# Kernel tuning notes

Measured on AMD Instinct MI355X. Metric: run time of the kernel, lower is better.

Reference implementation:

```python
import jax, jax.numpy as jnp
import numpy as np

N, E, G = 50000, 800000, 64
IN_C, HID, HEADS = 128, 64, 4
NEG_SLOPE = 0.2


def setup_inputs() -> dict:
    key = jax.random.key(0)
    ks = jax.random.split(key, 16)
    s = 0.05  # modest init scale
    inp = {
        "x": jax.random.normal(ks[0], (N, IN_C), jnp.float32),
        "edge_index": jax.random.randint(ks[1], (2, E), 0, N, jnp.int64),
        "batch": jnp.sort(jax.random.randint(ks[2], (N,), 0, G, jnp.int64)),
        # GAT layer 1: IN_C -> HEADS*HID, concat heads
        "W1": jax.random.normal(ks[3], (IN_C, HEADS * HID), jnp.float32) * s,
        "att_src1": jax.random.normal(ks[4], (HEADS, HID), jnp.float32) * s,
        "att_dst1": jax.random.normal(ks[5], (HEADS, HID), jnp.float32) * s,
        "b1": jnp.zeros((HEADS * HID,), jnp.float32),
        # GAT layer 2: HEADS*HID -> HID, 1 head
        "W2": jax.random.normal(ks[6], (HEADS * HID, HID), jnp.float32) * s,
        "att_src2": jax.random.normal(ks[7], (1, HID), jnp.float32) * s,
        "att_dst2": jax.random.normal(ks[8], (1, HID), jnp.float32) * s,
        "b2": jnp.zeros((HID,), jnp.float32),
        # MLP head
        "lin1_w": jax.random.normal(ks[9], (HID, 128), jnp.float32) * s,
        "lin1_b": jnp.zeros((128,), jnp.float32),
        "lin2_w": jax.random.normal(ks[10], (128, 1), jnp.float32) * s,
        "lin2_b": jnp.zeros((1,), jnp.float32),
    }
    return inp


def gat_layer(x, W, a_src, a_dst, b, src, dst, heads, ch):
    n = x.shape[0]
    h = (x @ W).reshape(n, heads, ch)                       # [N,H,C]
    alpha_src = jnp.sum(h * a_src, axis=-1)                 # [N,H]
    alpha_dst = jnp.sum(h * a_dst, axis=-1)                 # [N,H]
    e = alpha_src[src] + alpha_dst[dst]                     # [E',H] gather
    e = jax.nn.leaky_relu(e, NEG_SLOPE)
    # segment softmax over incoming edges of each dst node
    m = jax.ops.segment_max(e, dst, num_segments=n)         # [N,H]
    ex = jnp.exp(e - m[dst])
    denom = jax.ops.segment_sum(ex, dst, num_segments=n)    # [N,H]
    alpha = ex / (denom[dst] + 1e-16)                       # [E',H]
    msg = h[src] * alpha[:, :, None]                        # [E',H,C]
    out = jax.ops.segment_sum(msg, dst, num_segments=n)     # [N,H,C]
    return out.reshape(n, heads * ch) + b


def reference(x, W1, att_src1, att_dst1, b1, W2, att_src2, att_dst2, b2,
              lin1_w, lin1_b, lin2_w, lin2_b, edge_index, batch):
    # add self loops (PyG GATConv default)
    loops = jnp.arange(N, dtype=edge_index.dtype)
    src = jnp.concatenate([edge_index[0], loops])
    dst = jnp.concatenate([edge_index[1], loops])

    h = jax.nn.elu(gat_layer(x, W1, att_src1, att_dst1, b1, src, dst, HEADS, HID))
    h = jax.nn.elu(gat_layer(h, W2, att_src2, att_dst2, b2, src, dst, 1, HID))

    # global mean pool over graphs
    sums = jax.ops.segment_sum(h, batch, num_segments=G)    # [G,HID]
    cnt = jax.ops.segment_sum(jnp.ones((N,), h.dtype), batch, num_segments=G)
    pooled = sums / jnp.maximum(cnt, 1.0)[:, None]

    z = jax.nn.relu(pooled @ lin1_w + lin1_b)
    return (z @ lin2_w + lin2_b).squeeze(1)                 # [G]
```

## Files before the change

### kernel.cpp

```cpp
#include <hip/hip_runtime.h>
#include <hip/hip_bf16.h>
#include <math.h>

#define NN 50000
#define NE 800000
#define NG 64
#define INC 128
#define HIDC 64
#define NH 4
#define HC1 256
#define NEG 0.2f
#define NB 256
#define CE (NE/NB)
#define NW (NN/2)

static __device__ __forceinline__ float lrelu(float x){ return x > 0.f ? x : NEG*x; }
static __device__ __forceinline__ float eluf(float x){ return x > 0.f ? x : expm1f(x); }
static __device__ __forceinline__ unsigned short f2bf(float x){
    unsigned u = __float_as_uint(x);
    unsigned r = u + 0x7fffu + ((u>>16)&1u);
    return (unsigned short)(r>>16);
}
static __device__ __forceinline__ float bf2f(unsigned short b){
    return __uint_as_float(((unsigned)b) << 16);
}

__global__ __launch_bounds__(256) void k_hist(const int* __restrict__ ei, unsigned* __restrict__ hist)
{
    __shared__ unsigned h[NW];
    int tid = threadIdx.x, b = blockIdx.x;
    for (int w = tid; w < NW; w += 256) h[w] = 0u;
    __syncthreads();
    const int* dsts = ei + NE + b*CE;
    for (int i = tid; i < CE; i += 256){
        int d = dsts[i];
        atomicAdd(&h[d>>1], 1u << (16*(d&1)));
    }
    __syncthreads();
    unsigned* out = hist + (size_t)b*NW;
    for (int w = tid; w < NW; w += 256) out[w] = h[w];
}

__global__ __launch_bounds__(256) void k_colscan(const unsigned* __restrict__ hist,
                                                 unsigned short* __restrict__ bases,
                                                 int* __restrict__ deg)
{
    int n = blockIdx.x*256 + threadIdx.x;
    if (n >= NN) return;
    int w = n>>1, sh = 16*(n&1);
    unsigned run = 0;
    #pragma unroll 8
    for (int b = 0; b < NB; b++){
        unsigned c = (hist[(size_t)b*NW + w] >> sh) & 0xffffu;
        bases[(size_t)b*NN + n] = (unsigned short)run;
        run += c;
    }
    deg[n] = (int)run;
}

__global__ void k_scanA(const int* __restrict__ cnt, int* __restrict__ offs, int* __restrict__ bsum)
{
    __shared__ int s[256];
    int t = threadIdx.x;
    int i = blockIdx.x*256 + t;
    int v = (i < NN) ? cnt[i] : 0;
    s[t] = v; __syncthreads();
    #pragma unroll
    for (int d=1; d<256; d<<=1){
        int tv = (t>=d)? s[t-d] : 0; __syncthreads();
        s[t] += tv; __syncthreads();
    }
    if (i < NN) offs[i] = s[t] - v;
    if (t == 255) bsum[blockIdx.x] = s[255];
}

__global__ void k_scanB(int* __restrict__ bsum, int nb)
{
    __shared__ int s[256];
    int t = threadIdx.x;
    int v = (t < nb) ? bsum[t] : 0;
    s[t] = v; __syncthreads();
    #pragma unroll
    for (int d=1; d<256; d<<=1){
        int tv = (t>=d)? s[t-d] : 0; __syncthreads();
        s[t] += tv; __syncthreads();
    }
    if (t < nb) bsum[t] = s[t] - v;
}

__global__ void k_scanC(const int* __restrict__ bsum, int* __restrict__ offs)
{
    int t = threadIdx.x;
    int i = blockIdx.x*256 + t;
    if (i < NN) offs[i] += bsum[blockIdx.x];
    if (i == 0 && blockIdx.x == 0) offs[NN] = NE;
}

__global__ __launch_bounds__(256) void k_place(const int* __restrict__ ei,
                                               const int* __restrict__ offs,
                                               const unsigned short* __restrict__ bases,
                                               int* __restrict__ csr)
{
    __shared__ unsigned h[NW];
    int tid = threadIdx.x, b = blockIdx.x;
    for (int w = tid; w < NW; w += 256) h[w] = 0u;
    __syncthreads();
    const int* srcs = ei + b*CE;
    const int* dsts = ei + NE + b*CE;
    const unsigned short* myb = bases + (size_t)b*NN;
    for (int i = tid; i < CE; i += 256){
        int s = srcs[i], d = dsts[i];
        unsigned old = atomicAdd(&h[d>>1], 1u << (16*(d&1)));
        unsigned rank = (old >> (16*(d&1))) & 0xffffu;
        csr[(unsigned)offs[d] + (unsigned)myb[d] + rank] = s;
    }
}

__global__ __launch_bounds__(256) void k_gemm1(
    const float* __restrict__ x, const float* __restrict__ W1,
    const float* __restrict__ aw_s, const float* __restrict__ aw_d,
    unsigned short* __restrict__ h1b, float* __restrict__ as1, float* __restrict__ ad1)
{
    __shared__ float Al[64][68];
    __shared__ float Bl[64][128];
    int tid = threadIdx.x;
    int r0 = blockIdx.x * 64;
    int c0 = blockIdx.y * 128;
    float acc[8][4];
    #pragma unroll
    for (int i=0;i<8;i++){
        #pragma unroll
        for (int j=0;j<4;j++) acc[i][j]=0.f;
    }

    for (int k0 = 0; k0 < INC; k0 += 64) {
        {
            int row = tid>>2, q = tid&3;
            int gr = r0 + row; if (gr >= NN) gr = NN-1;
            const float4* srcp = (const float4*)(x + (size_t)gr*INC + k0 + q*16);
            float4* dstp = (float4*)(&Al[row][q*16]);
            #pragma unroll
            for (int j=0;j<4;j++) dstp[j] = srcp[j];
        }
        {
            int kk = tid>>5, f = tid&31;
            #pragma unroll
            for (int p=0;p<8;p++){
                int k = kk + p*8;
                ((float4*)(&Bl[k][0]))[f] = ((const float4*)(W1 + (size_t)(k0+k)*HC1 + c0))[f];
            }
        }
        __syncthreads();
        int rg = tid>>5, cg = tid&31;
        #pragma unroll 4
        for (int k=0;k<64;k++){
            float4 b = ((const float4*)(&Bl[k][0]))[cg];
            #pragma unroll
            for (int i=0;i<8;i++){
                float a = Al[rg*8+i][k];
                acc[i][0] = fmaf(a, b.x, acc[i][0]);
                acc[i][1] = fmaf(a, b.y, acc[i][1]);
                acc[i][2] = fmaf(a, b.z, acc[i][2]);
                acc[i][3] = fmaf(a, b.w, acc[i][3]);
            }
        }
        __syncthreads();
    }
    int rg = tid>>5, cg = tid&31;
    int cbase = c0 + cg*4;
    int head = cbase >> 6;
    int cw = cbase & 63;
    float4 wsv = *(const float4*)(aw_s + head*HIDC + cw);
    float4 wdv = *(const float4*)(aw_d + head*HIDC + cw);
    #pragma unroll
    for (int i=0;i<8;i++){
        int gr = r0 + rg*8 + i;
        bool ok = gr < NN;
        float4 c4; c4.x=acc[i][0]; c4.y=acc[i][1]; c4.z=acc[i][2]; c4.w=acc[i][3];
        if (ok){
            ushort4 hb;
            hb.x = f2bf(c4.x); hb.y = f2bf(c4.y); hb.z = f2bf(c4.z); hb.w = f2bf(c4.w);
            *(ushort4*)(h1b + (size_t)gr*HC1 + cbase) = hb;
        }
        float ps = c4.x*wsv.x + c4.y*wsv.y + c4.z*wsv.z + c4.w*wsv.w;
        float pd = c4.x*wdv.x + c4.y*wdv.y + c4.z*wdv.z + c4.w*wdv.w;
        #pragma unroll
        for (int d=1; d<16; d<<=1){
            ps += __shfl_xor(ps, d);
            pd += __shfl_xor(pd, d);
        }
        if (((cg & 15) == 0) && ok){
            as1[gr*4 + head] = ps;
            ad1[gr*4 + head] = pd;
        }
    }
}

__global__ __launch_bounds__(256) void k_agg1(
    const unsigned short* __restrict__ h1b, const float* __restrict__ as1, const float* __restrict__ ad1,
    const float* __restrict__ b1, const int* __restrict__ offs, const int* __restrict__ csr,
    float* __restrict__ h1o)
{
    int node = blockIdx.x*4 + (threadIdx.x>>6);
    if (node >= NN) return;
    int lane = threadIdx.x & 63;
    int hd = lane >> 4;
    float adv_l = ad1[node*4 + (lane&3)];
    const char* hp = (const char*)h1b;
    int lb = lane*8;
    float4 acc; acc.x=acc.y=acc.z=acc.w=0.f;
    float psum_l = 0.f;
    int base = offs[node], end = offs[node+1];
    for (int pos = base; pos < end; pos += 64){
        int nchunk = end - pos; if (nchunk > 64) nchunk = 64;
        int boff_l = ((lane < nchunk) ? csr[pos + lane] : 0) << 9;
        for (int sc = 0; sc*16 < nchunk; sc++){
            int srcv_off = __shfl(boff_l, sc*16 + (lane>>2));
            float p_l = 0.f;
            if (sc*16 + (lane>>2) < nchunk){
                float asv = as1[(srcv_off >> 7) + (lane&3)];
                p_l = expf(lrelu(asv + adv_l));
            }
            psum_l += p_l;
            int m = nchunk - sc*16; if (m > 16) m = 16;
            if (m == 16){
                #pragma unroll
                for (int j=0;j<16;j++){
                    int so = __shfl(boff_l, sc*16 + j);
                    float pj = __shfl(p_l, 4*j + hd);
                    ushort4 hb = *(const ushort4*)(hp + so + lb);
                    acc.x = fmaf(pj, bf2f(hb.x), acc.x);
                    acc.y = fmaf(pj, bf2f(hb.y), acc.y);
                    acc.z = fmaf(pj, bf2f(hb.z), acc.z);
                    acc.w = fmaf(pj, bf2f(hb.w), acc.w);
                }
            } else {
                for (int j=0;j<m;j++){
                    int so = __shfl(boff_l, sc*16 + j);
                    float pj = __shfl(p_l, 4*j + hd);
                    ushort4 hb = *(const ushort4*)(hp + so + lb);
                    acc.x = fmaf(pj, bf2f(hb.x), acc.x);
                    acc.y = fmaf(pj, bf2f(hb.y), acc.y);
                    acc.z = fmaf(pj, bf2f(hb.z), acc.z);
                    acc.w = fmaf(pj, bf2f(hb.w), acc.w);
                }
            }
        }
    }
    float s = psum_l;
    s += __shfl_xor(s, 4); s += __shfl_xor(s, 8);
    s += __shfl_xor(s, 16); s += __shfl_xor(s, 32);
    float ssum = __shfl(s, hd);
    {
        float p = expf(lrelu(as1[node*4 + hd] + ad1[node*4 + hd]));
        ssum += p;
        ushort4 hb = *(const ushort4*)(hp + (node << 9) + lb);
        acc.x = fmaf(p, bf2f(hb.x), acc.x);
        acc.y = fmaf(p, bf2f(hb.y), acc.y);
        acc.z = fmaf(p, bf2f(hb.z), acc.z);
        acc.w = fmaf(p, bf2f(hb.w), acc.w);
    }
    float inv = 1.f/(ssum + 1e-16f);
    float4 bv = ((const float4*)b1)[lane];
    float4 o;
    o.x = eluf(fmaf(acc.x, inv, bv.x));
    o.y = eluf(fmaf(acc.y, inv, bv.y));
    o.z = eluf(fmaf(acc.z, inv, bv.z));
    o.w = eluf(fmaf(acc.w, inv, bv.w));
    ((float4*)h1o)[(size_t)node*64 + lane] = o;
}

__global__ __launch_bounds__(256) void k_gemm2(
    const float* __restrict__ h1o, const float* __restrict__ W2,
    const float* __restrict__ aw_s, const float* __restrict__ aw_d,
    unsigned short* __restrict__ h2b, float* __restrict__ as2, float* __restrict__ ad2)
{
    __shared__ float Al[64][68];
    __shared__ float Bl[64][64];
    int tid = threadIdx.x;
    int r0 = blockIdx.x * 64;
    float acc[4][4];
    #pragma unroll
    for (int i=0;i<4;i++){
        #pragma unroll
        for (int j=0;j<4;j++) acc[i][j]=0.f;
    }

    for (int k0 = 0; k0 < HC1; k0 += 64) {
        {
            int row = tid>>2, q = tid&3;
            int gr = r0 + row; if (gr >= NN) gr = NN-1;
            const float4* srcp = (const float4*)(h1o + (size_t)gr*HC1 + k0 + q*16);
            float4* dstp = (float4*)(&Al[row][q*16]);
            #pragma unroll
            for (int j=0;j<4;j++) dstp[j] = srcp[j];
        }
        {
            int kk = tid>>4, f = tid&15;
            #pragma unroll
            for (int p=0;p<4;p++){
                int k = kk + p*16;
                ((float4*)(&Bl[k][0]))[f] = ((const float4*)(W2 + (size_t)(k0+k)*HIDC))[f];
            }
        }
        __syncthreads();
        int rg = tid>>4, cg = tid&15;
        #pragma unroll 4
        for (int k=0;k<64;k++){
            float4 b = ((const float4*)(&Bl[k][0]))[cg];
            #pragma unroll
            for (int i=0;i<4;i++){
                float a = Al[rg*4+i][k];
                acc[i][0] = fmaf(a, b.x, acc[i][0]);
                acc[i][1] = fmaf(a, b.y, acc[i][1]);
                acc[i][2] = fmaf(a, b.z, acc[i][2]);
                acc[i][3] = fmaf(a, b.w, acc[i][3]);
            }
        }
        __syncthreads();
    }
    int rg = tid>>4, cg = tid&15;
    float4 wsv = ((const float4*)aw_s)[cg];
    float4 wdv = ((const float4*)aw_d)[cg];
    #pragma unroll
    for (int i=0;i<4;i++){
        int gr = r0 + rg*4 + i;
        bool ok = gr < NN;
        float4 c4; c4.x=acc[i][0]; c4.y=acc[i][1]; c4.z=acc[i][2]; c4.w=acc[i][3];
        if (ok){
            ushort4 hb;
            hb.x = f2bf(c4.x); hb.y = f2bf(c4.y); hb.z = f2bf(c4.z); hb.w = f2bf(c4.w);
            *(ushort4*)(h2b + (size_t)gr*HIDC + cg*4) = hb;
        }
        float ps = c4.x*wsv.x + c4.y*wsv.y + c4.z*wsv.z + c4.w*wsv.w;
        float pd = c4.x*wdv.x + c4.y*wdv.y + c4.z*wdv.z + c4.w*wdv.w;
        #pragma unroll
        for (int d=1; d<16; d<<=1){
            ps += __shfl_xor(ps, d);
            pd += __shfl_xor(pd, d);
        }
        if (cg == 0 && ok){
            as2[gr] = ps;
            ad2[gr] = pd;
        }
    }
}

__global__ __launch_bounds__(256) void k_agg2(
    const unsigned short* __restrict__ h2b, const float* __restrict__ as2, const float* __restrict__ ad2,
    const float* __restrict__ b2, const int* __restrict__ offs, const int* __restrict__ csr,
    const int* __restrict__ batch, float* __restrict__ pool)
{
    __shared__ float pacc[4][64];
    __shared__ int gs[4];
    int tid = threadIdx.x;
    int wid = tid >> 6;
    int lane = tid & 63;
    int node = blockIdx.x*4 + wid;
    float adv = ad2[node];
    const char* hp = (const char*)h2b;
    int lb = lane*2;
    float accv = 0.f, psum_l = 0.f;
    int base = offs[node], end = offs[node+1];
    for (int pos = base; pos < end; pos += 64){
        int nchunk = end - pos; if (nchunk > 64) nchunk = 64;
        int boff_l = 0; float p_l = 0.f;
        if (lane < nchunk){
            int src_l = csr[pos + lane];
            boff_l = src_l << 7;
            p_l = expf(lrelu(as2[src_l] + adv));
        }
        psum_l += p_l;
        for (int sc = 0; sc*16 < nchunk; sc++){
            int m = nchunk - sc*16; if (m > 16) m = 16;
            if (m == 16){
                #pragma unroll
                for (int j=0;j<16;j++){
                    int jj = sc*16 + j;
                    int so = __shfl(boff_l, jj);
                    float pj = __shfl(p_l, jj);
                    accv = fmaf(pj, bf2f(*(const unsigned short*)(hp + so + lb)), accv);
                }
            } else {
                for (int j=0;j<m;j++){
                    int jj = sc*16 + j;
                    int so = __shfl(boff_l, jj);
                    float pj = __shfl(p_l, jj);
                    accv = fmaf(pj, bf2f(*(const unsigned short*)(hp + so + lb)), accv);
                }
            }
        }
    }
    float ssum = psum_l;
    ssum += __shfl_xor(ssum, 1); ssum += __shfl_xor(ssum, 2);
    ssum += __shfl_xor(ssum, 4); ssum += __shfl_xor(ssum, 8);
    ssum += __shfl_xor(ssum, 16); ssum += __shfl_xor(ssum, 32);
    {
        float p = expf(lrelu(as2[node] + adv));
        ssum += p;
        accv = fmaf(p, bf2f(*(const unsigned short*)(hp + (node << 7) + lb)), accv);
    }
    float o = eluf(accv/(ssum + 1e-16f) + b2[lane]);
    int g = batch[node];
    pacc[wid][lane] = o;
    if (lane == 0) gs[wid] = g;
    __syncthreads();
    if (gs[0] == gs[1] && gs[1] == gs[2] && gs[2] == gs[3]){
        if (wid == 0){
            float s = (pacc[0][lane] + pacc[1][lane]) + (pacc[2][lane] + pacc[3][lane]);
            atomicAdd(&pool[g*HIDC + lane], s);
        }
    } else {
        atomicAdd(&pool[g*HIDC + lane], o);
    }
}

__global__ __launch_bounds__(128) void k_mlp(
    const float* __restrict__ pool, const int* __restrict__ batch,
    const float* __restrict__ l1w, const float* __restrict__ l1b,
    const float* __restrict__ l2w, const float* __restrict__ l2b,
    float* __restrict__ out)
{
    __shared__ float pl[64];
    __shared__ float wsum[2];
    int g = blockIdx.x, t = threadIdx.x;
    int lo = 0, hi = NN;
    while (lo < hi){ int mid = (lo+hi)>>1; if (batch[mid] < g) lo = mid+1; else hi = mid; }
    int a = lo;
    lo = 0; hi = NN;
    while (lo < hi){ int mid = (lo+hi)>>1; if (batch[mid] < g+1) lo = mid+1; else hi = mid; }
    float inv = 1.f / fmaxf((float)(lo - a), 1.f);
    if (t < 64) pl[t] = pool[g*64 + t] * inv;
    __syncthreads();
    float z = l1b[t];
    #pragma unroll 8
    for (int c=0;c<64;c++) z = fmaf(pl[c], l1w[c*128 + t], z);
    z = fmaxf(z, 0.f);
    float part = z * l2w[t];
    #pragma unroll
    for (int d=1; d<64; d<<=1) part += __shfl_xor(part, d);
    if ((t & 63) == 0) wsum[t>>6] = part;
    __syncthreads();
    if (t == 0) out[g] = wsum[0] + wsum[1] + l2b[0];
}

extern "C" void kernel_launch(void* const* d_in, const int* in_sizes, int n_in,
                              void* d_out, int out_size, void* d_ws, size_t ws_size,
                              hipStream_t stream) {
    const float* x    = (const float*)d_in[0];
    const int*   ei   = (const int*)d_in[1];
    const int*   batch= (const int*)d_in[2];
    const float* W1   = (const float*)d_in[3];
    const float* as1w = (const float*)d_in[4];
    const float* ad1w = (const float*)d_in[5];
    const float* b1   = (const float*)d_in[6];
    const float* W2   = (const float*)d_in[7];
    const float* as2w = (const float*)d_in[8];
    const float* ad2w = (const float*)d_in[9];
    const float* b2   = (const float*)d_in[10];
    const float* l1w  = (const float*)d_in[11];
    const float* l1b  = (const float*)d_in[12];
    const float* l2w  = (const float*)d_in[13];
    const float* l2b  = (const float*)d_in[14];
    float* out = (float*)d_out;

    char* ws = (char*)d_ws;
    size_t off = 0;
    auto alloc = [&](size_t bytes) -> void* {
        void* p = ws + off; off += (bytes + 255) & ~(size_t)255; return p;
    };
    unsigned short* h1b = (unsigned short*)alloc((size_t)NN*HC1*2);
    float* h1o  = (float*)alloc((size_t)NN*HC1*4);
    unsigned short* h2b = (unsigned short*)h1b;
    unsigned* hist = (unsigned*)h1o;
    unsigned short* bases = (unsigned short*)((char*)h1o + (size_t)NB*NW*4);
    float* as1  = (float*)alloc((size_t)NN*4*4);
    float* ad1  = (float*)alloc((size_t)NN*4*4);
    float* as2  = (float*)alloc((size_t)NN*4);
    float* ad2  = (float*)alloc((size_t)NN*4);
    int*   deg  = (int*)alloc((size_t)NN*4);
    float* pool = (float*)alloc((size_t)NG*HIDC*4);
    int*   offs = (int*)alloc((size_t)(NN+16)*4);
    int*   bsum = (int*)alloc((size_t)256*4);
    int*   csr  = (int*)alloc((size_t)NE*4);
    (void)ws_size; (void)in_sizes; (void)n_in; (void)out_size;

    hipMemsetAsync(pool, 0, (size_t)NG*HIDC*4, stream);

    dim3 b256(256);
    int nb = (NN + 255)/256;
    k_hist   <<<dim3(NB), b256, 0, stream>>>(ei, hist);
    k_colscan<<<dim3(nb), b256, 0, stream>>>(hist, bases, deg);
    k_scanA  <<<dim3(nb), b256, 0, stream>>>(deg, offs, bsum);
    k_scanB  <<<dim3(1), b256, 0, stream>>>(bsum, nb);
    k_scanC  <<<dim3(nb), b256, 0, stream>>>(bsum, offs);
    k_place  <<<dim3(NB), b256, 0, stream>>>(ei, offs, bases, csr);
    k_gemm1  <<<dim3((NN+63)/64, 2), b256, 0, stream>>>(x, W1, as1w, ad1w, h1b, as1, ad1);
    k_agg1   <<<dim3((NN+3)/4), b256, 0, stream>>>(h1b, as1, ad1, b1, offs, csr, h1o);
    k_gemm2  <<<dim3((NN+63)/64), b256, 0, stream>>>(h1o, W2, as2w, ad2w, h2b, as2, ad2);
    k_agg2   <<<dim3((NN+3)/4), b256, 0, stream>>>(h2b, as2, ad2, b2, offs, csr, batch, pool);
    k_mlp    <<<dim3(NG), dim3(128), 0, stream>>>(pool, batch, l1w, l1b, l2w, l2b, out);
}
```

Baseline: 365.8 us.

## Replace FP32 shared-memory GEMMs with bf16 MFMA kernels using pre-transposed weights

Both dense projections switch from LDS-tiled FP32 FMA loops to per-wave 16x16x32 bf16 MFMA instructions. Activations are converted to bf16 in registers and fragments are loaded straight from global memory. A new small kernel converts and transposes W1 and W2 to bf16 each call so B fragments can be read contiguously. The change removes shared-memory staging and the FP32 ALU bottleneck, at the cost of reduced input precision, uncoalesced scalar bf16 output stores, and an extra launch.

```diff
diff --git a/kernel.cpp b/kernel.cpp
--- a/kernel.cpp
+++ b/kernel.cpp
@@ -14,6 +14,9 @@
 #define CE (NE/NB)
 #define NW (NN/2)
 
+typedef __attribute__((ext_vector_type(8))) short bf16x8;
+typedef __attribute__((ext_vector_type(4))) float f32x4;
+
 static __device__ __forceinline__ float lrelu(float x){ return x > 0.f ? x : NEG*x; }
 static __device__ __forceinline__ float eluf(float x){ return x > 0.f ? x : expm1f(x); }
 static __device__ __forceinline__ unsigned short f2bf(float x){
@@ -23,6 +26,14 @@
 }
 static __device__ __forceinline__ float bf2f(unsigned short b){
     return __uint_as_float(((unsigned)b) << 16);
+}
+
+__global__ __launch_bounds__(256) void k_prepw(const float* __restrict__ W1, const float* __restrict__ W2,
+                                               unsigned short* __restrict__ W1T, unsigned short* __restrict__ W2T)
+{
+    int i = blockIdx.x*256 + threadIdx.x;
+    if (i < INC*HC1){ int k = i / HC1, n = i % HC1; W1T[n*INC + k] = f2bf(W1[i]); }
+    if (i < HC1*HIDC){ int k = i / HIDC, n = i % HIDC; W2T[n*HC1 + k] = f2bf(W2[i]); }
 }
 
 __global__ __launch_bounds__(256) void k_hist(const int* __restrict__ ei, unsigned* __restrict__ hist)
@@ -116,82 +127,57 @@
     }
 }
 
-__global__ __launch_bounds__(256) void k_gemm1(
-    const float* __restrict__ x, const float* __restrict__ W1,
+__global__ __launch_bounds__(256) void k_gemm1m(
+    const float* __restrict__ x, const unsigned short* __restrict__ W1T,
     const float* __restrict__ aw_s, const float* __restrict__ aw_d,
     unsigned short* __restrict__ h1b, float* __restrict__ as1, float* __restrict__ ad1)
 {
-    __shared__ float Al[64][68];
-    __shared__ float Bl[64][128];
-    int tid = threadIdx.x;
-    int r0 = blockIdx.x * 64;
-    int c0 = blockIdx.y * 128;
-    float acc[8][4];
-    #pragma unroll
-    for (int i=0;i<8;i++){
+    int w = threadIdx.x >> 6, lane = threadIdx.x & 63;
+    int r0 = blockIdx.x*64 + w*16;
+    int l15 = lane & 15, lk = (lane >> 4)*8;
+    int arow = r0 + l15;
+    int la = arow < NN ? arow : NN-1;
+    const float* ap = x + (size_t)la*INC + lk;
+    const unsigned short* bt = W1T + l15*INC + lk;
+    f32x4 acc[16];
+    #pragma unroll
+    for (int t=0;t<16;t++){ acc[t][0]=0.f; acc[t][1]=0.f; acc[t][2]=0.f; acc[t][3]=0.f; }
+    #pragma unroll
+    for (int kc = 0; kc < 4; kc++){
+        float4 a01 = *(const float4*)(ap + kc*32);
+        float4 a23 = *(const float4*)(ap + kc*32 + 4);
+        bf16x8 af;
+        af[0]=(short)f2bf(a01.x); af[1]=(short)f2bf(a01.y);
+        af[2]=(short)f2bf(a01.z); af[3]=(short)f2bf(a01.w);
+        af[4]=(short)f2bf(a23.x); af[5]=(short)f2bf(a23.y);
+        af[6]=(short)f2bf(a23.z); af[7]=(short)f2bf(a23.w);
         #pragma unroll
-        for (int j=0;j<4;j++) acc[i][j]=0.f;
-    }
-
-    for (int k0 = 0; k0 < INC; k0 += 64) {
-        {
-            int row = tid>>2, q = tid&3;
-            int gr = r0 + row; if (gr >= NN) gr = NN-1;
-            const float4* srcp = (const float4*)(x + (size_t)gr*INC + k0 + q*16);
-            float4* dstp = (float4*)(&Al[row][q*16]);
-            #pragma unroll
-            for (int j=0;j<4;j++) dstp[j] = srcp[j];
-        }
-        {
-            int kk = tid>>5, f = tid&31;
-            #pragma unroll
-            for (int p=0;p<8;p++){
-                int k = kk + p*8;
-                ((float4*)(&Bl[k][0]))[f] = ((const float4*)(W1 + (size_t)(k0+k)*HC1 + c0))[f];
-            }
-        }
-        __syncthreads();
-        int rg = tid>>5, cg = tid&31;
-        #pragma unroll 4
-        for (int k=0;k<64;k++){
-            float4 b = ((const float4*)(&Bl[k][0]))[cg];
-            #pragma unroll
-            for (int i=0;i<8;i++){
-                float a = Al[rg*8+i][k];
-                acc[i][0] = fmaf(a, b.x, acc[i][0]);
-                acc[i][1] = fmaf(a, b.y, acc[i][1]);
-                acc[i][2] = fmaf(a, b.z, acc[i][2]);
-                acc[i][3] = fmaf(a, b.w, acc[i][3]);
-            }
-        }
-        __syncthreads();
-    }
-    int rg = tid>>5, cg = tid&31;
-    int cbase = c0 + cg*4;
-    int head = cbase >> 6;
-    int cw = cbase & 63;
-    float4 wsv = *(const float4*)(aw_s + head*HIDC + cw);
-    float4 wdv = *(const float4*)(aw_d + head*HIDC + cw);
-    #pragma unroll
-    for (int i=0;i<8;i++){
-        int gr = r0 + rg*8 + i;
-        bool ok = gr < NN;
-        float4 c4; c4.x=acc[i][0]; c4.y=acc[i][1]; c4.z=acc[i][2]; c4.w=acc[i][3];
-        if (ok){
-            ushort4 hb;
-            hb.x = f2bf(c4.x); hb.y = f2bf(c4.y); hb.z = f2bf(c4.z); hb.w = f2bf(c4.w);
-            *(ushort4*)(h1b + (size_t)gr*HC1 + cbase) = hb;
-        }
-        float ps = c4.x*wsv.x + c4.y*wsv.y + c4.z*wsv.z + c4.w*wsv.w;
-        float pd = c4.x*wdv.x + c4.y*wdv.y + c4.z*wdv.z + c4.w*wdv.w;
+        for (int nt = 0; nt < 16; nt++){
+            bf16x8 bfr = *(const bf16x8*)(bt + nt*16*INC + kc*32);
+            acc[nt] = __builtin_amdgcn_mfma_f32_16x16x32_bf16(af, bfr, acc[nt], 0, 0, 0);
+        }
+    }
+    int g = lane >> 4;
+    int crow0 = r0 + g*4;
+    #pragma unroll
+    for (int r = 0; r < 4; r++){
+        int row = crow0 + r;
+        bool ok = row < NN;
+        float ps[4] = {0.f,0.f,0.f,0.f}, pd[4] = {0.f,0.f,0.f,0.f};
         #pragma unroll
-        for (int d=1; d<16; d<<=1){
-            ps += __shfl_xor(ps, d);
-            pd += __shfl_xor(pd, d);
-        }
-        if (((cg & 15) == 0) && ok){
-            as1[gr*4 + head] = ps;
-            ad1[gr*4 + head] = pd;
+        for (int nt = 0; nt < 16; nt++){
+            int col = nt*16 + l15;
+            float v = acc[nt][r];
+            if (ok) h1b[(size_t)row*HC1 + col] = f2bf(v);
+            ps[nt>>2] += v * aw_s[col];
+            pd[nt>>2] += v * aw_d[col];
+        }
+        #pragma unroll
+        for (int h = 0; h < 4; h++){
+            float s = ps[h], d = pd[h];
+            s += __shfl_xor(s,1); s += __shfl_xor(s,2); s += __shfl_xor(s,4); s += __shfl_xor(s,8);
+            d += __shfl_xor(d,1); d += __shfl_xor(d,2); d += __shfl_xor(d,4); d += __shfl_xor(d,8);
+            if (ok && l15 == 0){ as1[row*4 + h] = s; ad1[row*4 + h] = d; }
         }
     }
 }
@@ -270,79 +256,54 @@
     ((float4*)h1o)[(size_t)node*64 + lane] = o;
 }
 
-__global__ __launch_bounds__(256) void k_gemm2(
-    const float* __restrict__ h1o, const float* __restrict__ W2,
+__global__ __launch_bounds__(256) void k_gemm2m(
+    const float* __restrict__ h1o, const unsigned short* __restrict__ W2T,
     const float* __restrict__ aw_s, const float* __restrict__ aw_d,
     unsigned short* __restrict__ h2b, float* __restrict__ as2, float* __restrict__ ad2)
 {
-    __shared__ float Al[64][68];
-    __shared__ float Bl[64][64];
-    int tid = threadIdx.x;
-    int r0 = blockIdx.x * 64;
-    float acc[4][4];
-    #pragma unroll
-    for (int i=0;i<4;i++){
+    int w = threadIdx.x >> 6, lane = threadIdx.x & 63;
+    int r0 = blockIdx.x*64 + w*16;
+    int l15 = lane & 15, lk = (lane >> 4)*8;
+    int arow = r0 + l15;
+    int la = arow < NN ? arow : NN-1;
+    const float* ap = h1o + (size_t)la*HC1 + lk;
+    const unsigned short* bt = W2T + l15*HC1 + lk;
+    f32x4 acc[4];
+    #pragma unroll
+    for (int t=0;t<4;t++){ acc[t][0]=0.f; acc[t][1]=0.f; acc[t][2]=0.f; acc[t][3]=0.f; }
+    #pragma unroll
+    for (int kc = 0; kc < 8; kc++){
+        float4 a01 = *(const float4*)(ap + kc*32);
+        float4 a23 = *(const float4*)(ap + kc*32 + 4);
+        bf16x8 af;
+        af[0]=(short)f2bf(a01.x); af[1]=(short)f2bf(a01.y);
+        af[2]=(short)f2bf(a01.z); af[3]=(short)f2bf(a01.w);
+        af[4]=(short)f2bf(a23.x); af[5]=(short)f2bf(a23.y);
+        af[6]=(short)f2bf(a23.z); af[7]=(short)f2bf(a23.w);
         #pragma unroll
-        for (int j=0;j<4;j++) acc[i][j]=0.f;
-    }
-
-    for (int k0 = 0; k0 < HC1; k0 += 64) {
-        {
-            int row = tid>>2, q = tid&3;
-            int gr = r0 + row; if (gr >= NN) gr = NN-1;
-            const float4* srcp = (const float4*)(h1o + (size_t)gr*HC1 + k0 + q*16);
-            float4* dstp = (float4*)(&Al[row][q*16]);
-            #pragma unroll
-            for (int j=0;j<4;j++) dstp[j] = srcp[j];
-        }
-        {
-            int kk = tid>>4, f = tid&15;
-            #pragma unroll
-            for (int p=0;p<4;p++){
-                int k = kk + p*16;
-                ((float4*)(&Bl[k][0]))[f] = ((const float4*)(W2 + (size_t)(k0+k)*HIDC))[f];
-            }
-        }
-        __syncthreads();
-        int rg = tid>>4, cg = tid&15;
-        #pragma unroll 4
-        for (int k=0;k<64;k++){
-            float4 b = ((const float4*)(&Bl[k][0]))[cg];
-            #pragma unroll
-            for (int i=0;i<4;i++){
-                float a = Al[rg*4+i][k];
-                acc[i][0] = fmaf(a, b.x, acc[i][0]);
-                acc[i][1] = fmaf(a, b.y, acc[i][1]);
-                acc[i][2] = fmaf(a, b.z, acc[i][2]);
-                acc[i][3] = fmaf(a, b.w, acc[i][3]);
-            }
-        }
-        __syncthreads();
-    }
-    int rg = tid>>4, cg = tid&15;
-    float4 wsv = ((const float4*)aw_s)[cg];
-    float4 wdv = ((const float4*)aw_d)[cg];
-    #pragma unroll
-    for (int i=0;i<4;i++){
-        int gr = r0 + rg*4 + i;
-        bool ok = gr < NN;
-        float4 c4; c4.x=acc[i][0]; c4.y=acc[i][1]; c4.z=acc[i][2]; c4.w=acc[i][3];
-        if (ok){
-            ushort4 hb;
-            hb.x = f2bf(c4.x); hb.y = f2bf(c4.y); hb.z = f2bf(c4.z); hb.w = f2bf(c4.w);
-            *(ushort4*)(h2b + (size_t)gr*HIDC + cg*4) = hb;
-        }
-        float ps = c4.x*wsv.x + c4.y*wsv.y + c4.z*wsv.z + c4.w*wsv.w;
-        float pd = c4.x*wdv.x + c4.y*wdv.y + c4.z*wdv.z + c4.w*wdv.w;
+        for (int nt = 0; nt < 4; nt++){
+            bf16x8 bfr = *(const bf16x8*)(bt + nt*16*HC1 + kc*32);
+            acc[nt] = __builtin_amdgcn_mfma_f32_16x16x32_bf16(af, bfr, acc[nt], 0, 0, 0);
+        }
+    }
+    int g = lane >> 4;
+    int crow0 = r0 + g*4;
+    #pragma unroll
+    for (int r = 0; r < 4; r++){
+        int row = crow0 + r;
+        bool ok = row < NN;
+        float ps = 0.f, pd = 0.f;
         #pragma unroll
-        for (int d=1; d<16; d<<=1){
-            ps += __shfl_xor(ps, d);
-            pd += __shfl_xor(pd, d);
-        }
-        if (cg == 0 && ok){
-            as2[gr] = ps;
-            ad2[gr] = pd;
-        }
+        for (int nt = 0; nt < 4; nt++){
+            int col = nt*16 + l15;
+            float v = acc[nt][r];
+            if (ok) h2b[(size_t)row*HIDC + col] = f2bf(v);
+            ps += v * aw_s[col];
+            pd += v * aw_d[col];
+        }
+        ps += __shfl_xor(ps,1); ps += __shfl_xor(ps,2); ps += __shfl_xor(ps,4); ps += __shfl_xor(ps,8);
+        pd += __shfl_xor(pd,1); pd += __shfl_xor(pd,2); pd += __shfl_xor(pd,4); pd += __shfl_xor(pd,8);
+        if (ok && l15 == 0){ as2[row] = ps; ad2[row] = pd; }
     }
 }
 
@@ -483,21 +444,24 @@
     int*   offs = (int*)alloc((size_t)(NN+16)*4);
     int*   bsum = (int*)alloc((size_t)256*4);
     int*   csr  = (int*)alloc((size_t)NE*4);
+    unsigned short* W1T = (unsigned short*)alloc((size_t)HC1*INC*2);
+    unsigned short* W2T = (unsigned short*)alloc((size_t)HIDC*HC1*2);
     (void)ws_size; (void)in_sizes; (void)n_in; (void)out_size;
 
     hipMemsetAsync(pool, 0, (size_t)NG*HIDC*4, stream);
 
     dim3 b256(256);
     int nb = (NN + 255)/256;
+    k_prepw  <<<dim3(128), b256, 0, stream>>>(W1, W2, W1T, W2T);
     k_hist   <<<dim3(NB), b256, 0, stream>>>(ei, hist);
     k_colscan<<<dim3(nb), b256, 0, stream>>>(hist, bases, deg);
     k_scanA  <<<dim3(nb), b256, 0, stream>>>(deg, offs, bsum);
     k_scanB  <<<dim3(1), b256, 0, stream>>>(bsum, nb);
     k_scanC  <<<dim3(nb), b256, 0, stream>>>(bsum, offs);
     k_place  <<<dim3(NB), b256, 0, stream>>>(ei, offs, bases, csr);
-    k_gemm1  <<<dim3((NN+63)/64, 2), b256, 0, stream>>>(x, W1, as1w, ad1w, h1b, as1, ad1);
+    k_gemm1m <<<dim3((NN+63)/64), b256, 0, stream>>>(x, W1T, as1w, ad1w, h1b, as1, ad1);
     k_agg1   <<<dim3((NN+3)/4), b256, 0, stream>>>(h1b, as1, ad1, b1, offs, csr, h1o);
-    k_gemm2  <<<dim3((NN+63)/64), b256, 0, stream>>>(h1o, W2, as2w, ad2w, h2b, as2, ad2);
+    k_gemm2m <<<dim3((NN+63)/64), b256, 0, stream>>>(h1o, W2T, as2w, ad2w, h2b, as2, ad2);
     k_agg2   <<<dim3((NN+3)/4), b256, 0, stream>>>(h2b, as2, ad2, b2, offs, csr, batch, pool);
     k_mlp    <<<dim3(NG), dim3(128), 0, stream>>>(pool, batch, l1w, l1b, l2w, l2b, out);
 }
```

Result: faster. 358.4 us (-2.0%).
